# Optimization experiments

Hardware: AMD Instinct MI355X
Metric: run time of the kernel (lower is better)

## Reference

```python
import jax, jax.numpy as jnp
import numpy as np

V = 32          # number_variables
DEG = 12        # degree
ORDER = 3       # spline_order (cubic)
N_BASIS = DEG + ORDER - 1  # 14, rows of params
LO, HI = -15.0, 15.0       # polynomial_range[:, 0]
EPS = 1e-6


def make_knots():
    dist = (HI - LO) / (DEG - 1)
    k = DEG + 2 * ORDER
    return jnp.linspace(LO - ORDER * dist, HI + ORDER * dist, k, dtype=jnp.float32)


def bspline_basis(x, knots, order):
    # x: [N, P] -> basis: [N, P, N_BASIS] via Cox-de Boor recursion (Naive_Basis)
    xk = x[..., None]
    b = ((xk >= knots[:-1]) & (xk < knots[1:])).astype(x.dtype)  # degree-0, [N,P,K-1]
    t = knots
    for k in range(1, order + 1):
        left = (xk - t[:-(k + 1)]) / (t[k:-1] - t[:-(k + 1)])
        right = (t[k + 1:] - xk) / (t[k + 1:] - t[1:-k])
        b = left * b[..., :-1] + right * b[..., 1:]
    return b  # [N, P, K-1-order] == [N, P, N_BASIS]


def setup_inputs() -> dict:
    key = jax.random.key(0)
    k1, k2 = jax.random.split(key)
    num_lambdas = V * (V - 1) // 2  # 496
    inp = jax.random.normal(k1, (16384, V), dtype=jnp.float32)
    log_d = jnp.zeros((16384, V), dtype=jnp.float32)
    params = 0.001 * jnp.ones((N_BASIS, num_lambdas), dtype=jnp.float32)
    return {"input": inp, "log_d": log_d, "params": params}


def reference(input, log_d, params):
    n = input.shape[0]
    knots = make_knots()
    rows, cols = np.tril_indices(V, -1)  # matches torch.tril_indices(V, V, offset=-1)
    rows = jnp.asarray(rows); cols = jnp.asarray(cols)
    # clamp into half-open spline support for valid degree-0 basis
    x = jnp.clip(input, LO, HI - EPS)
    xs = x[:, cols]                                  # [N, P] per-pair covariate values
    basis = bspline_basis(xs, knots, ORDER)          # [N, P, N_BASIS]
    lam = jnp.einsum('npk,kp->np', basis, params)    # [N, P] lambda values
    # lower-triangular lambda matrix: identity + strict lower entries
    lm = jnp.broadcast_to(jnp.eye(V, dtype=input.dtype), (n, V, V))
    lm = lm.at[:, rows, cols].set(lam)
    out = jnp.einsum('nvc,nc->nv', lm, input)        # bmm(lambda_matrix, input)
    # ridge penalties on spline coefficients (penalize_towards=0)
    d2 = jnp.diff(params, n=2, axis=0)
    d1 = jnp.diff(params, n=1, axis=0)
    second_pen = jnp.sum(d2 ** 2)
    first_pen = jnp.sum(d1 ** 2)
    param_pen = jnp.sum(params ** 2)
    return out, lm, second_pen, first_pen, param_pen
```

## Files before the change

kernel.cpp:

```cpp
#include <hip/hip_runtime.h>

#define VDIM   32
#define NPAIR  496
#define NBASIS 14
#define NPARAM (NBASIS * NPAIR)
#define NINT   11
#define ROWS   8
#define LROW   544

typedef float f32x4 __attribute__((ext_vector_type(4)));

__device__ __forceinline__ int seg_of(int v) {
    int m = v - 1;
    if (m <= 0) return 0;
    int q = m >> 2, r = m & 3;
    return 4 * (2 * q * (q + 1) + r * (q + 1));
}

__global__ __launch_bounds__(256) void Decorrelation_prep(
    const float* __restrict__ params,
    f32x4* __restrict__ ptv,
    float* __restrict__ pens)
{
    const int tid = threadIdx.x;
    const int b   = blockIdx.x;
    if (b < NINT) {
        const int i = b;
        for (int p = tid; p < NPAIR; p += 256) {
            f32x4 w = { params[(i    ) * NPAIR + p],
                        params[(i + 1) * NPAIR + p],
                        params[(i + 2) * NPAIR + p],
                        params[(i + 3) * NPAIR + p] };
            ptv[i * NPAIR + p] = w;
        }
    } else {
        float s2 = 0.f, s1 = 0.f, sp = 0.f;
        for (int idx = tid; idx < NPARAM; idx += 256) {
            const float a = params[idx];
            sp += a * a;
            if (idx < NPARAM - NPAIR) {
                const float bb = params[idx + NPAIR];
                const float d1 = bb - a;
                s1 += d1 * d1;
                if (idx < NPARAM - 2 * NPAIR) {
                    const float cc = params[idx + 2 * NPAIR];
                    const float d2 = cc - 2.f * bb + a;
                    s2 += d2 * d2;
                }
            }
        }
        #pragma unroll
        for (int off = 32; off > 0; off >>= 1) {
            s2 += __shfl_down(s2, off);
            s1 += __shfl_down(s1, off);
            sp += __shfl_down(sp, off);
        }
        __shared__ float ws[3][4];
        const int lane = tid & 63, wid = tid >> 6;
        if (lane == 0) { ws[0][wid] = s2; ws[1][wid] = s1; ws[2][wid] = sp; }
        __syncthreads();
        if (tid == 0) {
            pens[0] = ws[0][0] + ws[0][1] + ws[0][2] + ws[0][3];
            pens[1] = ws[1][0] + ws[1][1] + ws[1][2] + ws[1][3];
            pens[2] = ws[2][0] + ws[2][1] + ws[2][2] + ws[2][3];
        }
    }
}

__global__ __launch_bounds__(256, 4) void Decorrelation_35270271435435_kernel(
    const float* __restrict__ input,
    const f32x4* __restrict__ ptv,
    float* __restrict__ out,
    float* __restrict__ lm,
    int N)
{
    __shared__ float lam[ROWS][LROW];

    const int tid = threadIdx.x;
    const int n0  = blockIdx.x * ROWS;

    const int p1 = tid;
    int v1 = (int)((1.0f + sqrtf(8.0f * (float)p1 + 1.0f)) * 0.5f);
    while (v1 * (v1 - 1) / 2 > p1) --v1;
    while ((v1 + 1) * v1 / 2 <= p1) ++v1;
    const int c1 = p1 - v1 * (v1 - 1) / 2;
    const int o1 = seg_of(v1) + c1;

    const int  p2   = tid + 256;
    const bool has2 = (p2 < NPAIR);
    int c2 = 0, o2 = 0;
    if (has2) {
        int v2 = (int)((1.0f + sqrtf(8.0f * (float)p2 + 1.0f)) * 0.5f);
        while (v2 * (v2 - 1) / 2 > p2) --v2;
        while ((v2 + 1) * v2 / 2 <= p2) ++v2;
        c2 = p2 - v2 * (v2 - 1) / 2;
        o2 = seg_of(v2) + c2;
    }

    const float dist  = 30.0f / 11.0f;
    const float invd  = 11.0f / 30.0f;
    const float t0    = -15.0f - 3.0f * dist;
    const float sixth = 1.0f / 6.0f;

    #pragma unroll 4
    for (int r = 0; r < ROWS; ++r) {
        const int base = (n0 + r) * VDIM;
        {
            const float xi = input[base + c1];
            float x = fminf(fmaxf(xi, -15.0f), 15.0f - 1e-6f);
            float u = (x - t0) * invd;
            int   i = (int)floorf(u);
            i = min(13, max(3, i));
            const float uu  = u - (float)i;
            const float om  = 1.0f - uu;
            const float uu2 = uu * uu, uu3 = uu2 * uu;
            const float w0 = om * om * om * sixth;
            const float w1 = (3.0f * uu3 - 6.0f * uu2 + 4.0f) * sixth;
            const float w2 = (-3.0f * uu3 + 3.0f * uu2 + 3.0f * uu + 1.0f) * sixth;
            const float w3 = uu3 * sixth;
            const f32x4 q  = ptv[(i - 3) * NPAIR + p1];
            lam[r][o1] = w0 * q.x + w1 * q.y + w2 * q.z + w3 * q.w;
        }
        if (has2) {
            const float xi = input[base + c2];
            float x = fminf(fmaxf(xi, -15.0f), 15.0f - 1e-6f);
            float u = (x - t0) * invd;
            int   i = (int)floorf(u);
            i = min(13, max(3, i));
            const float uu  = u - (float)i;
            const float om  = 1.0f - uu;
            const float uu2 = uu * uu, uu3 = uu2 * uu;
            const float w0 = om * om * om * sixth;
            const float w1 = (3.0f * uu3 - 6.0f * uu2 + 4.0f) * sixth;
            const float w2 = (-3.0f * uu3 + 3.0f * uu2 + 3.0f * uu + 1.0f) * sixth;
            const float w3 = uu3 * sixth;
            const f32x4 q  = ptv[(i - 3) * NPAIR + p2];
            lam[r][o2] = w0 * q.x + w1 * q.y + w2 * q.z + w3 * q.w;
        }
    }
    __syncthreads();

    const int v    = tid >> 3;
    const int c0   = (tid & 7) << 2;
    const int segv = seg_of(v);
    float* lmp = lm + (size_t)n0 * (VDIM * VDIM) + tid * 4;

    #pragma unroll
    for (int r = 0; r < ROWS; ++r, lmp += VDIM * VDIM) {
        const int n = n0 + r;
        const f32x4 lq = *(const f32x4*)&lam[r][segv + c0];
        const f32x4 xq = *(const f32x4*)(input + n * VDIM + c0);
        float vals[4];
        float partial = 0.0f;
        #pragma unroll
        for (int j = 0; j < 4; ++j) {
            const int c = c0 + j;
            const float lv = (j == 0) ? lq.x : (j == 1) ? lq.y : (j == 2) ? lq.z : lq.w;
            const float xv = (j == 0) ? xq.x : (j == 1) ? xq.y : (j == 2) ? xq.z : xq.w;
            const float val = (c < v) ? lv : ((c == v) ? 1.0f : 0.0f);
            vals[j] = val;
            partial += val * xv;
        }
        f32x4 f4 = { vals[0], vals[1], vals[2], vals[3] };
        __builtin_nontemporal_store(f4, (f32x4*)lmp);

        partial += __shfl_down(partial, 4, 8);
        partial += __shfl_down(partial, 2, 8);
        partial += __shfl_down(partial, 1, 8);
        if ((tid & 7) == 0) out[n * VDIM + v] = partial;
    }
}

extern "C" void kernel_launch(void* const* d_in, const int* in_sizes, int n_in,
                              void* d_out, int out_size, void* d_ws, size_t ws_size,
                              hipStream_t stream) {
    const float* input  = (const float*)d_in[0];
    const float* params = (const float*)d_in[2];
    const int N = in_sizes[0] / VDIM;

    float* out  = (float*)d_out;
    float* lm   = out + (size_t)N * VDIM;
    float* pens = lm + (size_t)N * VDIM * VDIM;

    f32x4* ptv = (f32x4*)d_ws;

    Decorrelation_prep<<<NINT + 1, 256, 0, stream>>>(params, ptv, pens);

    const int nb = (N + ROWS - 1) / ROWS;
    Decorrelation_35270271435435_kernel<<<nb, 256, 0, stream>>>(
        input, ptv, out, lm, N);
}
```

Baseline: 103.2 us.

## Assign two rows per wave to drop block barrier and use plain stores

Restructures the kernel so each wave owns two batch rows: the wave computes all 496 lambda values for its rows into shared memory and then immediately writes the lambda matrix and output for those same rows. Because no wave reads another wave's data, the block-wide __syncthreads is removed. The lambda-matrix stores become regular stores instead of nontemporal ones, and launch bounds ask for 6 blocks per CU. The trade-off is 8 per-lane index precomputations held in registers, some redundant lanes for the padded pairs, and the loss of the nontemporal hint on a large write-only stream.

```diff
diff --git a/kernel.cpp b/kernel.cpp
--- a/kernel.cpp
+++ b/kernel.cpp
@@ -67,7 +67,7 @@
     }
 }
 
-__global__ __launch_bounds__(256, 4) void Decorrelation_35270271435435_kernel(
+__global__ __launch_bounds__(256, 6) void Decorrelation_35270271435435_kernel(
     const float* __restrict__ input,
     const f32x4* __restrict__ ptv,
     float* __restrict__ out,
@@ -76,25 +76,23 @@
 {
     __shared__ float lam[ROWS][LROW];
 
-    const int tid = threadIdx.x;
-    const int n0  = blockIdx.x * ROWS;
+    const int tid  = threadIdx.x;
+    const int wave = tid >> 6;
+    const int lane = tid & 63;
+    const int n0   = blockIdx.x * ROWS;
 
-    const int p1 = tid;
-    int v1 = (int)((1.0f + sqrtf(8.0f * (float)p1 + 1.0f)) * 0.5f);
-    while (v1 * (v1 - 1) / 2 > p1) --v1;
-    while ((v1 + 1) * v1 / 2 <= p1) ++v1;
-    const int c1 = p1 - v1 * (v1 - 1) / 2;
-    const int o1 = seg_of(v1) + c1;
-
-    const int  p2   = tid + 256;
-    const bool has2 = (p2 < NPAIR);
-    int c2 = 0, o2 = 0;
-    if (has2) {
-        int v2 = (int)((1.0f + sqrtf(8.0f * (float)p2 + 1.0f)) * 0.5f);
-        while (v2 * (v2 - 1) / 2 > p2) --v2;
-        while ((v2 + 1) * v2 / 2 <= p2) ++v2;
-        c2 = p2 - v2 * (v2 - 1) / 2;
-        o2 = seg_of(v2) + c2;
+    int  oo[8], cc[8], pp[8];
+    bool act[8];
+    #pragma unroll
+    for (int k = 0; k < 8; ++k) {
+        const int p = lane + 64 * k;
+        act[k] = (p < NPAIR);
+        const int pe = act[k] ? p : (NPAIR - 1);
+        int v = (int)((1.0f + sqrtf(8.0f * (float)pe + 1.0f)) * 0.5f);
+        while (v * (v - 1) / 2 > pe) --v;
+        while ((v + 1) * v / 2 <= pe) ++v;
+        const int c = pe - v * (v - 1) / 2;
+        pp[k] = pe; cc[k] = c; oo[k] = seg_of(v) + c;
     }
 
     const float dist  = 30.0f / 11.0f;
@@ -102,11 +100,15 @@
     const float t0    = -15.0f - 3.0f * dist;
     const float sixth = 1.0f / 6.0f;
 
-    #pragma unroll 4
-    for (int r = 0; r < ROWS; ++r) {
-        const int base = (n0 + r) * VDIM;
-        {
-            const float xi = input[base + c1];
+    #pragma unroll
+    for (int rr = 0; rr < 2; ++rr) {
+        const int r = wave * 2 + rr;
+        const int n = n0 + r;
+        if (n >= N) break;
+        const float* xrow = input + n * VDIM;
+        #pragma unroll
+        for (int k = 0; k < 8; ++k) {
+            const float xi = xrow[cc[k]];
             float x = fminf(fmaxf(xi, -15.0f), 15.0f - 1e-6f);
             float u = (x - t0) * invd;
             int   i = (int)floorf(u);
@@ -118,56 +120,44 @@
             const float w1 = (3.0f * uu3 - 6.0f * uu2 + 4.0f) * sixth;
             const float w2 = (-3.0f * uu3 + 3.0f * uu2 + 3.0f * uu + 1.0f) * sixth;
             const float w3 = uu3 * sixth;
-            const f32x4 q  = ptv[(i - 3) * NPAIR + p1];
-            lam[r][o1] = w0 * q.x + w1 * q.y + w2 * q.z + w3 * q.w;
-        }
-        if (has2) {
-            const float xi = input[base + c2];
-            float x = fminf(fmaxf(xi, -15.0f), 15.0f - 1e-6f);
-            float u = (x - t0) * invd;
-            int   i = (int)floorf(u);
-            i = min(13, max(3, i));
-            const float uu  = u - (float)i;
-            const float om  = 1.0f - uu;
-            const float uu2 = uu * uu, uu3 = uu2 * uu;
-            const float w0 = om * om * om * sixth;
-            const float w1 = (3.0f * uu3 - 6.0f * uu2 + 4.0f) * sixth;
-            const float w2 = (-3.0f * uu3 + 3.0f * uu2 + 3.0f * uu + 1.0f) * sixth;
-            const float w3 = uu3 * sixth;
-            const f32x4 q  = ptv[(i - 3) * NPAIR + p2];
-            lam[r][o2] = w0 * q.x + w1 * q.y + w2 * q.z + w3 * q.w;
+            const f32x4 q  = ptv[(i - 3) * NPAIR + pp[k]];
+            const float lv = w0 * q.x + w1 * q.y + w2 * q.z + w3 * q.w;
+            if (act[k]) lam[r][oo[k]] = lv;
         }
     }
-    __syncthreads();
-
-    const int v    = tid >> 3;
-    const int c0   = (tid & 7) << 2;
-    const int segv = seg_of(v);
-    float* lmp = lm + (size_t)n0 * (VDIM * VDIM) + tid * 4;
 
     #pragma unroll
-    for (int r = 0; r < ROWS; ++r, lmp += VDIM * VDIM) {
+    for (int rr = 0; rr < 2; ++rr) {
+        const int r = wave * 2 + rr;
         const int n = n0 + r;
-        const f32x4 lq = *(const f32x4*)&lam[r][segv + c0];
-        const f32x4 xq = *(const f32x4*)(input + n * VDIM + c0);
-        float vals[4];
-        float partial = 0.0f;
+        if (n >= N) break;
+        const float* xrow  = input + n * VDIM;
+        float*       lmrow = lm + (size_t)n * (VDIM * VDIM);
         #pragma unroll
         for (int j = 0; j < 4; ++j) {
-            const int c = c0 + j;
-            const float lv = (j == 0) ? lq.x : (j == 1) ? lq.y : (j == 2) ? lq.z : lq.w;
-            const float xv = (j == 0) ? xq.x : (j == 1) ? xq.y : (j == 2) ? xq.z : xq.w;
-            const float val = (c < v) ? lv : ((c == v) ? 1.0f : 0.0f);
-            vals[j] = val;
-            partial += val * xv;
+            const int v  = j * 8 + (lane >> 3);
+            const int c0 = (lane & 7) << 2;
+            const f32x4 lq = *(const f32x4*)&lam[r][seg_of(v) + c0];
+            const f32x4 xq = *(const f32x4*)(xrow + c0);
+            float vals[4];
+            float partial = 0.0f;
+            #pragma unroll
+            for (int t = 0; t < 4; ++t) {
+                const int c = c0 + t;
+                const float lv = (t == 0) ? lq.x : (t == 1) ? lq.y : (t == 2) ? lq.z : lq.w;
+                const float xv = (t == 0) ? xq.x : (t == 1) ? xq.y : (t == 2) ? xq.z : xq.w;
+                const float val = (c < v) ? lv : ((c == v) ? 1.0f : 0.0f);
+                vals[t] = val;
+                partial += val * xv;
+            }
+            f32x4 f4 = { vals[0], vals[1], vals[2], vals[3] };
+            *(f32x4*)(lmrow + j * 256 + lane * 4) = f4;
+
+            partial += __shfl_down(partial, 4, 8);
+            partial += __shfl_down(partial, 2, 8);
+            partial += __shfl_down(partial, 1, 8);
+            if ((lane & 7) == 0) out[n * VDIM + v] = partial;
         }
-        f32x4 f4 = { vals[0], vals[1], vals[2], vals[3] };
-        __builtin_nontemporal_store(f4, (f32x4*)lmp);
-
-        partial += __shfl_down(partial, 4, 8);
-        partial += __shfl_down(partial, 2, 8);
-        partial += __shfl_down(partial, 1, 8);
-        if ((tid & 7) == 0) out[n * VDIM + v] = partial;
     }
 }
 
```

After: 102.4 us. No clear change (-0.7%).
